# Performance work log

Measured on AMD Instinct MI355X. Metric: run time of the kernel, lower is better.

## Reference

```python
import jax, jax.numpy as jnp
import numpy as np

LN_EPS = 1e-5


def setup_inputs() -> dict:
    key = jax.random.key(0)
    ks = jax.random.split(key, 8)
    N, H, E, D, B = 262144, 768, 768, 2048, 65536
    return {
        "u_t": jax.random.normal(ks[0], (B, E), dtype=jnp.float32),
        "s_i": jax.random.randint(ks[1], (B,), 0, N, dtype=jnp.int64),
        "speaker_embeddings": jax.random.normal(ks[2], (N, H), dtype=jnp.float32),
        "W1": jax.random.normal(ks[3], (D, H + E), dtype=jnp.float32) * 0.02,
        "b1": jax.random.normal(ks[4], (D,), dtype=jnp.float32) * 0.02,
        "W2": jax.random.normal(ks[5], (H, D), dtype=jnp.float32) * 0.02,
        "b2": jax.random.normal(ks[6], (H,), dtype=jnp.float32) * 0.02,
        "ln_gamma": jnp.ones((H,), dtype=jnp.float32),
        "ln_beta": jnp.zeros((H,), dtype=jnp.float32),
    }


def reference(u_t, s_i, speaker_embeddings, W1, b1, W2, b2, ln_gamma, ln_beta):
    # gather speaker vectors: [B, H]
    h_t = speaker_embeddings[s_i]
    # concat [u_t, h_t] along features: [B, E+H]
    x = jnp.concatenate([u_t, h_t], axis=-1)
    # Linear -> GELU (exact, torch default) -> (Dropout=identity in eval)
    h = jax.nn.gelu(jnp.einsum("bf,df->bd", x, W1) + b1, approximate=False)
    # Linear -> (Dropout=identity) : [B, H]
    y = jnp.einsum("bd,hd->bh", h, W2) + b2
    # LayerNorm over last dim
    mu = jnp.mean(y, axis=-1, keepdims=True)
    var = jnp.mean((y - mu) ** 2, axis=-1, keepdims=True)
    new_h_t = (y - mu) * jax.lax.rsqrt(var + LN_EPS) * ln_gamma + ln_beta
    # scatter-add back into the memory table (duplicates accumulate)
    updated = speaker_embeddings.at[s_i].add(new_h_t)
    return new_h_t, updated
```

## Files before the change

### kernel.cpp

```cpp
#include <hip/hip_runtime.h>
#include <hip/hip_bf16.h>

typedef unsigned short u16;
typedef unsigned int u32;
typedef short bf16x8 __attribute__((ext_vector_type(8)));
typedef float f32x4 __attribute__((ext_vector_type(4)));

#define BAR() asm volatile("s_barrier" ::: "memory")
#define WAITV4() asm volatile("s_waitcnt vmcnt(4)" ::: "memory")
#define WAITV0() asm volatile("s_waitcnt vmcnt(0)" ::: "memory")
#define WAITL() asm volatile("s_waitcnt lgkmcnt(0)" ::: "memory")

__device__ __forceinline__ unsigned pk2(float lo, float hi) {
    unsigned a = (unsigned)__builtin_bit_cast(u16, __float2bfloat16(lo));
    unsigned b = (unsigned)__builtin_bit_cast(u16, __float2bfloat16(hi));
    return a | (b << 16);
}
__device__ __forceinline__ u16 f2bf(float v) {
    return __builtin_bit_cast(u16, __float2bfloat16(v));
}
__device__ __forceinline__ void gl_lds16(const u16* g, u16* l) {
    __builtin_amdgcn_global_load_lds(
        (const __attribute__((address_space(1))) u32*)g,
        (__attribute__((address_space(3))) u32*)l, 16, 0, 0);
}

__global__ void cvtbf(const float4* __restrict__ s, uint2* __restrict__ d, int n4) {
    int i = blockIdx.x * blockDim.x + threadIdx.x;
    int stride = gridDim.x * blockDim.x;
    for (; i < n4; i += stride) {
        float4 f = s[i];
        uint2 o;
        o.x = pk2(f.x, f.y);
        o.y = pk2(f.z, f.w);
        d[i] = o;
    }
}

__global__ __launch_bounds__(256) void xbuild(const float* __restrict__ u_t,
                                              const float* __restrict__ emb,
                                              const int* __restrict__ s_i,
                                              u16* __restrict__ xb) {
    const long u = (long)blockIdx.x * blockDim.x + threadIdx.x;
    const int row = (int)(u / 192);
    const int c8 = (int)(u % 192);
    const float* src = (c8 < 96) ? (u_t + (long)row * 768 + c8 * 8)
                                 : (emb + (long)s_i[row] * 768 + (c8 - 96) * 8);
    float4 f0 = ((const float4*)src)[0];
    float4 f1 = ((const float4*)src)[1];
    uint4 o;
    o.x = pk2(f0.x, f0.y);
    o.y = pk2(f0.z, f0.w);
    o.z = pk2(f1.x, f1.y);
    o.w = pk2(f1.z, f1.w);
    *(uint4*)(xb + u * 8) = o;
}

template <int LDK, int NT, int TN, int EPI>
__global__ __launch_bounds__(512, 2) void gemm256(
    const u16* __restrict__ Ag, const u16* __restrict__ Bg,
    const float* __restrict__ bias, u16* __restrict__ outb,
    float* __restrict__ outf) {
    __shared__ __align__(16) u16 lds[65536];

    const int tid = threadIdx.x;
    const int lane = tid & 63;
    const int wv = tid >> 6;
    const int wm = wv >> 2;
    const int wn = wv & 3;

    const int cpx = (int)gridDim.x >> 3;
    const int tile = ((int)blockIdx.x & 7) * cpx + ((int)blockIdx.x >> 3);
    const int tm = tile / TN, tn = tile % TN;
    const long rowBase = (long)tm * 256;
    const long colBase = (long)tn * 256;

    const int srow = tid >> 2;
    const int gch = (tid & 3) ^ ((tid >> 3) & 3);
    const u16* pA = Ag + (rowBase + srow) * (long)LDK + gch * 8;
    const u16* pB = Bg + (colBase + srow) * (long)LDK + gch * 8;
    const int dstBase = wv * 512;

    auto stageA = [&](int kt, int ks, int b) {
        const u16* s = pA + kt * 64 + ks * 32;
        u16* d = lds + b * 32768 + ks * 8192 + dstBase;
        gl_lds16(s, d);
        gl_lds16(s + (long)128 * LDK, d + 4096);
    };
    auto stageB = [&](int kt, int ks, int b) {
        const u16* s = pB + kt * 64 + ks * 32;
        u16* d = lds + b * 32768 + 16384 + ks * 8192 + dstBase;
        gl_lds16(s, d);
        gl_lds16(s + (long)128 * LDK, d + 4096);
    };

    const int l15 = lane & 15, lc = lane >> 4;
    int offA[8], offB[4];
#pragma unroll
    for (int i = 0; i < 8; ++i) {
        int r = wm * 128 + i * 16 + l15;
        offA[i] = r * 32 + ((lc ^ ((r >> 1) & 3)) << 3);
    }
#pragma unroll
    for (int n = 0; n < 4; ++n) {
        int r = wn * 64 + n * 16 + l15;
        offB[n] = r * 32 + ((lc ^ ((r >> 1) & 3)) << 3);
    }

    f32x4 acc[8][4];
    const f32x4 zero = {0.f, 0.f, 0.f, 0.f};
#pragma unroll
    for (int m = 0; m < 8; ++m)
#pragma unroll
        for (int n = 0; n < 4; ++n) acc[m][n] = zero;

    stageA(0, 0, 0);
    stageB(0, 0, 0);
    stageA(0, 1, 0);
    stageB(0, 1, 0);
    WAITV4();
    BAR();

    bf16x8 bA[4], bB[4];
    for (int kt = 0; kt < NT; ++kt) {
        const int b = kt & 1;
        const u16* rA0 = lds + b * 32768;
        const u16* rB0 = rA0 + 16384;
        const u16* rA1 = rA0 + 8192;
        const u16* rB1 = rB0 + 8192;
        const bool pf = (kt + 1 < NT);

#pragma unroll
        for (int n = 0; n < 4; ++n) bB[n] = *(const bf16x8*)(rB0 + offB[n]);
#pragma unroll
        for (int m = 0; m < 4; ++m) bA[m] = *(const bf16x8*)(rA0 + offA[m]);
        if (pf) stageA(kt + 1, 0, b ^ 1);
        BAR();
        WAITL();
        __builtin_amdgcn_s_setprio(1);
#pragma unroll
        for (int m = 0; m < 4; ++m)
#pragma unroll
            for (int n = 0; n < 4; ++n)
                acc[m][n] = __builtin_amdgcn_mfma_f32_16x16x32_bf16(bA[m], bB[n], acc[m][n], 0, 0, 0);
        __builtin_amdgcn_s_setprio(0);
        BAR();

#pragma unroll
        for (int m = 0; m < 4; ++m) bA[m] = *(const bf16x8*)(rA0 + offA[4 + m]);
        if (pf) stageB(kt + 1, 0, b ^ 1);
        BAR();
        WAITL();
        __builtin_amdgcn_s_setprio(1);
#pragma unroll
        for (int m = 0; m < 4; ++m)
#pragma unroll
            for (int n = 0; n < 4; ++n)
                acc[4 + m][n] = __builtin_amdgcn_mfma_f32_16x16x32_bf16(bA[m], bB[n], acc[4 + m][n], 0, 0, 0);
        __builtin_amdgcn_s_setprio(0);
        if (pf) { WAITV4(); } else { WAITV0(); }
        BAR();

#pragma unroll
        for (int n = 0; n < 4; ++n) bB[n] = *(const bf16x8*)(rB1 + offB[n]);
#pragma unroll
        for (int m = 0; m < 4; ++m) bA[m] = *(const bf16x8*)(rA1 + offA[m]);
        if (pf) stageA(kt + 1, 1, b ^ 1);
        BAR();
        WAITL();
        __builtin_amdgcn_s_setprio(1);
#pragma unroll
        for (int m = 0; m < 4; ++m)
#pragma unroll
            for (int n = 0; n < 4; ++n)
                acc[m][n] = __builtin_amdgcn_mfma_f32_16x16x32_bf16(bA[m], bB[n], acc[m][n], 0, 0, 0);
        __builtin_amdgcn_s_setprio(0);
        BAR();

#pragma unroll
        for (int m = 0; m < 4; ++m) bA[m] = *(const bf16x8*)(rA1 + offA[4 + m]);
        if (pf) stageB(kt + 1, 1, b ^ 1);
        BAR();
        WAITL();
        __builtin_amdgcn_s_setprio(1);
#pragma unroll
        for (int m = 0; m < 4; ++m)
#pragma unroll
            for (int n = 0; n < 4; ++n)
                acc[4 + m][n] = __builtin_amdgcn_mfma_f32_16x16x32_bf16(bA[m], bB[n], acc[4 + m][n], 0, 0, 0);
        __builtin_amdgcn_s_setprio(0);
        if (pf) { WAITV4(); } else { WAITV0(); }
        BAR();
    }

    const int N = TN * 256;
#pragma unroll
    for (int n = 0; n < 4; ++n) {
        long gc = colBase + wn * 64 + n * 16 + l15;
        float bv = bias[gc];
#pragma unroll
        for (int i = 0; i < 8; ++i) {
            long gr = rowBase + wm * 128 + i * 16 + (lc << 2);
#pragma unroll
            for (int j = 0; j < 4; ++j) {
                float v = acc[i][n][j] + bv;
                if constexpr (EPI == 0) {
                    v = 0.5f * v * (1.0f + erff(v * 0.70710678118f));
                    outb[(gr + j) * N + gc] = f2bf(v);
                } else {
                    outf[(gr + j) * N + gc] = v;
                }
            }
        }
    }
}

__global__ __launch_bounds__(256) void ln_scatter(float* __restrict__ y,
                                                  const float* __restrict__ gamma,
                                                  const float* __restrict__ beta,
                                                  const int* __restrict__ s_i,
                                                  float* __restrict__ upd) {
    const int lane = threadIdx.x & 63;
    const long row = (long)blockIdx.x * 4 + (threadIdx.x >> 6);
    const long base = row * 768;
    float v[12];
#pragma unroll
    for (int i = 0; i < 12; ++i) v[i] = y[base + i * 64 + lane];
    float s = 0.f, q = 0.f;
#pragma unroll
    for (int i = 0; i < 12; ++i) { s += v[i]; q += v[i] * v[i]; }
#pragma unroll
    for (int off = 32; off > 0; off >>= 1) {
        s += __shfl_xor(s, off, 64);
        q += __shfl_xor(q, off, 64);
    }
    const float mu = s * (1.f / 768.f);
    const float var = q * (1.f / 768.f) - mu * mu;
    const float inv = rsqrtf(var + 1e-5f);
    const long si = s_i[row];
#pragma unroll
    for (int i = 0; i < 12; ++i) {
        int c = i * 64 + lane;
        float r = (v[i] - mu) * inv * gamma[c] + beta[c];
        y[base + c] = r;
        atomicAdd(&upd[si * 768 + c], r);
    }
}

__global__ void copy4(const float4* __restrict__ s, float4* __restrict__ d, long n) {
    long i = (long)blockIdx.x * blockDim.x + threadIdx.x;
    long stride = (long)gridDim.x * blockDim.x;
    for (; i < n; i += stride) d[i] = s[i];
}

extern "C" void kernel_launch(void* const* d_in, const int* in_sizes, int n_in,
                              void* d_out, int out_size, void* d_ws, size_t ws_size,
                              hipStream_t stream) {
    const float* u_t = (const float*)d_in[0];
    const int* s_i = (const int*)d_in[1];
    const float* emb = (const float*)d_in[2];
    const float* W1 = (const float*)d_in[3];
    const float* b1 = (const float*)d_in[4];
    const float* W2 = (const float*)d_in[5];
    const float* b2 = (const float*)d_in[6];
    const float* gamma = (const float*)d_in[7];
    const float* beta = (const float*)d_in[8];

    float* out = (float*)d_out;
    float* newh = out;
    float* upd = out + 50331648L;

    u16* base = (u16*)upd;
    u16* hbuf = base;
    u16* xb = base + 134217728L;
    u16* w1b = base + 234881024L;
    u16* w2b = base + 238026752L;

    cvtbf<<<1024, 256, 0, stream>>>((const float4*)W1, (uint2*)w1b, 786432);
    cvtbf<<<1024, 256, 0, stream>>>((const float4*)W2, (uint2*)w2b, 393216);
    xbuild<<<49152, 256, 0, stream>>>(u_t, emb, s_i, xb);
    gemm256<1536, 24, 8, 0><<<2048, 512, 0, stream>>>(xb, w1b, b1, hbuf, nullptr);
    gemm256<2048, 32, 3, 1><<<768, 512, 0, stream>>>(hbuf, w2b, b2, nullptr, newh);
    copy4<<<2048, 256, 0, stream>>>((const float4*)emb, (float4*)upd, 50331648L);
    ln_scatter<<<16384, 256, 0, stream>>>(newh, gamma, beta, s_i, upd);
}
```

Measured before the change: 1.390 ms.

## Fold embedding table copy into GEMM grids and deepen LDS pipeline to 4 stages

Both GEMM kernels now reserve every 4th or 5th block for streaming part of the embedding table copy into the output, so that memory-bound copy overlaps with compute-bound MFMA blocks. The standalone copy shrinks to the remaining range, and the scratch buffers are rearranged so the copied regions do not overlap live bf16 data. The GEMM main loop moves from 2 stages of 64-wide K steps to 4 stages of 32-wide K steps with three loads in flight. Risks include copy blocks contending for bandwidth with GEMM loads, and the buffer placement having to avoid clobbering data that is still in use.

New measurement: 1.427 ms. 2.7% more time.

```diff
diff --git a/kernel.cpp b/kernel.cpp
--- a/kernel.cpp
+++ b/kernel.cpp
@@ -7,6 +7,7 @@
 typedef float f32x4 __attribute__((ext_vector_type(4)));
 
 #define BAR() asm volatile("s_barrier" ::: "memory")
+#define WAITV8() asm volatile("s_waitcnt vmcnt(8)" ::: "memory")
 #define WAITV4() asm volatile("s_waitcnt vmcnt(4)" ::: "memory")
 #define WAITV0() asm volatile("s_waitcnt vmcnt(0)" ::: "memory")
 #define WAITL() asm volatile("s_waitcnt lgkmcnt(0)" ::: "memory")
@@ -56,40 +57,51 @@
     *(uint4*)(xb + u * 8) = o;
 }
 
-template <int LDK, int NT, int TN, int EPI>
+template <int LDK, int NT, int TN, int EPI, int CMOD>
 __global__ __launch_bounds__(512, 2) void gemm256(
     const u16* __restrict__ Ag, const u16* __restrict__ Bg,
     const float* __restrict__ bias, u16* __restrict__ outb,
-    float* __restrict__ outf) {
+    float* __restrict__ outf, const float4* __restrict__ csrc,
+    float4* __restrict__ cdst, long ccount, int cstride) {
     __shared__ __align__(16) u16 lds[65536];
 
     const int tid = threadIdx.x;
+    const int nblk = (int)gridDim.x;
+    const int chunk = nblk >> 3;
+    const int swz = ((int)blockIdx.x & 7) * chunk + ((int)blockIdx.x >> 3);
+
+    if constexpr (CMOD > 0) {
+        if ((swz % CMOD) == CMOD - 1) {
+            long i = (long)(swz / CMOD) * 512 + tid;
+            for (; i < ccount; i += cstride) cdst[i] = csrc[i];
+            return;
+        }
+    }
+    const int tile = (CMOD > 0) ? (swz - swz / CMOD) : swz;
+    const int tm = tile / TN, tn = tile % TN;
+    const long rowBase = (long)tm * 256;
+    const long colBase = (long)tn * 256;
+
     const int lane = tid & 63;
     const int wv = tid >> 6;
     const int wm = wv >> 2;
     const int wn = wv & 3;
 
-    const int cpx = (int)gridDim.x >> 3;
-    const int tile = ((int)blockIdx.x & 7) * cpx + ((int)blockIdx.x >> 3);
-    const int tm = tile / TN, tn = tile % TN;
-    const long rowBase = (long)tm * 256;
-    const long colBase = (long)tn * 256;
-
     const int srow = tid >> 2;
-    const int gch = (tid & 3) ^ ((tid >> 3) & 3);
+    const int gch = (tid & 3) ^ ((srow >> 1) & 3);
     const u16* pA = Ag + (rowBase + srow) * (long)LDK + gch * 8;
     const u16* pB = Bg + (colBase + srow) * (long)LDK + gch * 8;
     const int dstBase = wv * 512;
 
-    auto stageA = [&](int kt, int ks, int b) {
-        const u16* s = pA + kt * 64 + ks * 32;
-        u16* d = lds + b * 32768 + ks * 8192 + dstBase;
+    auto stageA = [&](int kt, int b) {
+        const u16* s = pA + kt * 32;
+        u16* d = lds + b * 16384 + dstBase;
         gl_lds16(s, d);
         gl_lds16(s + (long)128 * LDK, d + 4096);
     };
-    auto stageB = [&](int kt, int ks, int b) {
-        const u16* s = pB + kt * 64 + ks * 32;
-        u16* d = lds + b * 32768 + 16384 + ks * 8192 + dstBase;
+    auto stageB = [&](int kt, int b) {
+        const u16* s = pB + kt * 32;
+        u16* d = lds + b * 16384 + 8192 + dstBase;
         gl_lds16(s, d);
         gl_lds16(s + (long)128 * LDK, d + 4096);
     };
@@ -114,27 +126,24 @@
 #pragma unroll
         for (int n = 0; n < 4; ++n) acc[m][n] = zero;
 
-    stageA(0, 0, 0);
-    stageB(0, 0, 0);
-    stageA(0, 1, 0);
-    stageB(0, 1, 0);
-    WAITV4();
+    stageA(0, 0); stageB(0, 0);
+    stageA(1, 1); stageB(1, 1);
+    stageA(2, 2); stageB(2, 2);
+    WAITV8();
     BAR();
 
     bf16x8 bA[4], bB[4];
     for (int kt = 0; kt < NT; ++kt) {
-        const int b = kt & 1;
-        const u16* rA0 = lds + b * 32768;
-        const u16* rB0 = rA0 + 16384;
-        const u16* rA1 = rA0 + 8192;
-        const u16* rB1 = rB0 + 8192;
-        const bool pf = (kt + 1 < NT);
-
-#pragma unroll
-        for (int n = 0; n < 4; ++n) bB[n] = *(const bf16x8*)(rB0 + offB[n]);
-#pragma unroll
-        for (int m = 0; m < 4; ++m) bA[m] = *(const bf16x8*)(rA0 + offA[m]);
-        if (pf) stageA(kt + 1, 0, b ^ 1);
+        const int b = kt & 3;
+        const u16* rA = lds + b * 16384;
+        const u16* rB = rA + 8192;
+        const bool pf = (kt + 3 < NT);
+
+#pragma unroll
+        for (int n = 0; n < 4; ++n) bB[n] = *(const bf16x8*)(rB + offB[n]);
+#pragma unroll
+        for (int m = 0; m < 4; ++m) bA[m] = *(const bf16x8*)(rA + offA[m]);
+        if (pf) stageA(kt + 3, (kt + 3) & 3);
         BAR();
         WAITL();
         __builtin_amdgcn_s_setprio(1);
@@ -147,8 +156,8 @@
         BAR();
 
 #pragma unroll
-        for (int m = 0; m < 4; ++m) bA[m] = *(const bf16x8*)(rA0 + offA[4 + m]);
-        if (pf) stageB(kt + 1, 0, b ^ 1);
+        for (int m = 0; m < 4; ++m) bA[m] = *(const bf16x8*)(rA + offA[4 + m]);
+        if (pf) stageB(kt + 3, (kt + 3) & 3);
         BAR();
         WAITL();
         __builtin_amdgcn_s_setprio(1);
@@ -158,38 +167,9 @@
             for (int n = 0; n < 4; ++n)
                 acc[4 + m][n] = __builtin_amdgcn_mfma_f32_16x16x32_bf16(bA[m], bB[n], acc[4 + m][n], 0, 0, 0);
         __builtin_amdgcn_s_setprio(0);
-        if (pf) { WAITV4(); } else { WAITV0(); }
-        BAR();
-
-#pragma unroll
-        for (int n = 0; n < 4; ++n) bB[n] = *(const bf16x8*)(rB1 + offB[n]);
-#pragma unroll
-        for (int m = 0; m < 4; ++m) bA[m] = *(const bf16x8*)(rA1 + offA[m]);
-        if (pf) stageA(kt + 1, 1, b ^ 1);
-        BAR();
-        WAITL();
-        __builtin_amdgcn_s_setprio(1);
-#pragma unroll
-        for (int m = 0; m < 4; ++m)
-#pragma unroll
-            for (int n = 0; n < 4; ++n)
-                acc[m][n] = __builtin_amdgcn_mfma_f32_16x16x32_bf16(bA[m], bB[n], acc[m][n], 0, 0, 0);
-        __builtin_amdgcn_s_setprio(0);
-        BAR();
-
-#pragma unroll
-        for (int m = 0; m < 4; ++m) bA[m] = *(const bf16x8*)(rA1 + offA[4 + m]);
-        if (pf) stageB(kt + 1, 1, b ^ 1);
-        BAR();
-        WAITL();
-        __builtin_amdgcn_s_setprio(1);
-#pragma unroll
-        for (int m = 0; m < 4; ++m)
-#pragma unroll
-            for (int n = 0; n < 4; ++n)
-                acc[4 + m][n] = __builtin_amdgcn_mfma_f32_16x16x32_bf16(bA[m], bB[n], acc[4 + m][n], 0, 0, 0);
-        __builtin_amdgcn_s_setprio(0);
-        if (pf) { WAITV4(); } else { WAITV0(); }
+        if (pf) { WAITV8(); }
+        else if (kt + 2 < NT) { WAITV4(); }
+        else { WAITV0(); }
         BAR();
     }
 
@@ -271,16 +251,23 @@
     float* upd = out + 50331648L;
 
     u16* base = (u16*)upd;
-    u16* hbuf = base;
-    u16* xb = base + 134217728L;
-    u16* w1b = base + 234881024L;
+    u16* xb = base;
+    u16* w1b = base + 100663296L;
+    u16* hbuf = base + 103809024L;
     u16* w2b = base + 238026752L;
+
+    const float4* embq = (const float4*)emb;
+    float4* updq = (float4*)upd;
 
     cvtbf<<<1024, 256, 0, stream>>>((const float4*)W1, (uint2*)w1b, 786432);
     cvtbf<<<1024, 256, 0, stream>>>((const float4*)W2, (uint2*)w2b, 393216);
     xbuild<<<49152, 256, 0, stream>>>(u_t, emb, s_i, xb);
-    gemm256<1536, 24, 8, 0><<<2048, 512, 0, stream>>>(xb, w1b, b1, hbuf, nullptr);
-    gemm256<2048, 32, 3, 1><<<768, 512, 0, stream>>>(hbuf, w2b, b2, nullptr, newh);
-    copy4<<<2048, 256, 0, stream>>>((const float4*)emb, (float4*)upd, 50331648L);
+    gemm256<1536, 48, 8, 0, 5><<<2560, 512, 0, stream>>>(
+        xb, w1b, b1, hbuf, nullptr,
+        embq + 29949952L, updq + 29949952L, 20381696L, 262144);
+    gemm256<2048, 64, 3, 1, 4><<<1024, 512, 0, stream>>>(
+        hbuf, w2b, b2, nullptr, newh,
+        embq, updq, 12976128L, 131072);
+    copy4<<<2048, 256, 0, stream>>>(embq + 12976128L, updq + 12976128L, 16973824L);
     ln_scatter<<<16384, 256, 0, stream>>>(newh, gamma, beta, s_i, upd);
 }
```
